# Performance work log

Measured on AMD Instinct MI355X. Metric: run time of the kernel, lower is better.

## Reference

```python
import jax, jax.numpy as jnp
import numpy as np

B, S, D = 4, 2048, 512
H, DK, DV = 8, 64, 64

def setup_inputs() -> dict:
    key = jax.random.key(0)
    ks = jax.random.split(key, 11)
    s = 0.02
    return {
        "q_in": jax.random.normal(ks[0], (B, S, D), jnp.float32),
        "k_in": jax.random.normal(ks[1], (B, S, D), jnp.float32),
        "v_in": jax.random.normal(ks[2], (B, S, D), jnp.float32),
        "Wq": jax.random.normal(ks[3], (H, D, DK), jnp.float32) * s,
        "bq": jax.random.normal(ks[4], (H, DK), jnp.float32) * s,
        "Wk": jax.random.normal(ks[5], (H, D, DK), jnp.float32) * s,
        "bk": jax.random.normal(ks[6], (H, DK), jnp.float32) * s,
        "Wv": jax.random.normal(ks[7], (H, D, DV), jnp.float32) * s,
        "bv": jax.random.normal(ks[8], (H, DV), jnp.float32) * s,
        "Wo": jax.random.normal(ks[9], (H * DV, D), jnp.float32) * s,
        "bo": jax.random.normal(ks[10], (D,), jnp.float32) * s,
    }


def reference(q_in, k_in, v_in, Wq, bq, Wk, bk, Wv, bv, Wo, bo):
    # Per-head Q/K/V projections, batched over heads (same math as the
    # original Python loop over SingleAttention heads).
    q = jnp.einsum("bsd,hdk->bhsk", q_in, Wq) + bq[None, :, None, :]   # [B,H,S,DK]
    k = jnp.einsum("bsd,hdk->bhsk", k_in, Wk) + bk[None, :, None, :]   # [B,H,S,DK]
    v = jnp.einsum("bsd,hdv->bhsv", v_in, Wv) + bv[None, :, None, :]   # [B,H,S,DV]
    scale = 1.0 / jnp.sqrt(jnp.float32(DK))
    scores = jnp.einsum("bhqk,bhsk->bhqs", q, k) * scale               # [B,H,S,S]
    attn = jax.nn.softmax(scores, axis=-1)
    out = jnp.einsum("bhqs,bhsv->bhqv", attn, v)                        # [B,H,S,DV]
    # concat heads along feature dim: [B,S,H*DV]
    concat = out.transpose(0, 2, 1, 3).reshape(B, S, H * DV)
    return concat @ Wo + bo                                             # [B,S,D]
```

## Files before the change

### kernel.cpp

```cpp
#include <hip/hip_runtime.h>
#include <hip/hip_bf16.h>

using bf16 = __hip_bfloat16;
typedef short short8  __attribute__((ext_vector_type(8)));
typedef short short4v __attribute__((ext_vector_type(4)));
typedef float float4v __attribute__((ext_vector_type(4)));
typedef float f32x16  __attribute__((ext_vector_type(16)));
typedef unsigned int uint4v __attribute__((ext_vector_type(4)));

#define MFMA_BF16   __builtin_amdgcn_mfma_f32_16x16x32_bf16
#define MFMA32_BF16 __builtin_amdgcn_mfma_f32_32x32x16_bf16

#define B_  4
#define S_  2048
#define D_  512
#define H_  8
#define DK_ 64


__device__ __forceinline__ short f2bf(float f) {
  bf16 h = __float2bfloat16(f);
  return *reinterpret_cast<short*>(&h);
}

__device__ __forceinline__ unsigned cvtpk(float lo, float hi) {
  unsigned r;
  asm("v_cvt_pk_bf16_f32 %0, %1, %2" : "=v"(r) : "v"(lo), "v"(hi));
  return r;
}

__device__ __forceinline__ void plswap(unsigned& a, unsigned& b) {
  asm("v_permlane32_swap_b32 %0, %1" : "+v"(a), "+v"(b));
}

__device__ __forceinline__ short8 mk8(unsigned v0, unsigned v1, unsigned v2,
                                      unsigned v3) {
  uint4v u;
  u[0] = v0; u[1] = v1; u[2] = v2; u[3] = v3;
  return __builtin_bit_cast(short8, u);
}

__global__ __launch_bounds__(256)
void transpose_w(const float* __restrict__ Wq, const float* __restrict__ Wk,
                 const float* __restrict__ Wv, const float* __restrict__ Wo,
                 short* __restrict__ WqT, short* __restrict__ WkT,
                 short* __restrict__ WvT, short* __restrict__ WoT) {
  __shared__ float tile[64 * 65];
  const int mat = blockIdx.y, t = blockIdx.x, tid = threadIdx.x;
  const float* W = (mat == 0) ? Wq : (mat == 1) ? Wk : (mat == 2) ? Wv : Wo;
  short* T       = (mat == 0) ? WqT : (mat == 1) ? WkT : (mat == 2) ? WvT : WoT;

  size_t sbase, ss, dbase;
  if (mat < 3) {
    int hh = t >> 3, d0 = (t & 7) * 64;
    sbase = (size_t)hh * 32768 + (size_t)d0 * 64;
    ss = 64;
    dbase = (size_t)hh * 64 * 512 + d0;
  } else {
    int n0 = (t >> 3) * 64, k0 = (t & 7) * 64;
    sbase = (size_t)k0 * 512 + n0;
    ss = 512;
    dbase = (size_t)n0 * 512 + k0;
  }

  {
    int r = tid >> 2, c0 = (tid & 3) * 16;
#pragma unroll
    for (int j = 0; j < 4; j++)
      *(float4v*)&tile[r * 65 + c0 + j * 4] =
          *(const float4v*)&W[sbase + (size_t)r * ss + c0 + j * 4];
  }
  __syncthreads();
  {
    int c = tid >> 2, r0 = (tid & 3) * 16;
#pragma unroll
    for (int j = 0; j < 2; j++) {
      short8 s;
#pragma unroll
      for (int u = 0; u < 8; u++) s[u] = f2bf(tile[(r0 + j * 8 + u) * 65 + c]);
      *(short8*)&T[dbase + (size_t)c * 512 + r0 + j * 8] = s;
    }
  }
}

__device__ __forceinline__ void gemm_core(const void* __restrict__ A,
                                          const short* __restrict__ Bt,
                                          int m0, int n0, int fp32,
                                          short* As, short* Bs,
                                          float4v acc[4][4]) {
  const int tid  = threadIdx.x;
  const int lane = tid & 63, wave = tid >> 6;
  const int quad = lane >> 4, l16 = lane & 15;
  const int wm = (wave >> 1) * 64, wn = (wave & 1) * 64;

  for (int k0 = 0; k0 < 512; k0 += 64) {
    __syncthreads();
    if (fp32) {
      const float* Af = (const float*)A;
#pragma unroll
      for (int i = 0; i < 4; i++) {
        int cid = tid + 256 * i;
        int row = cid >> 3, kc = (cid & 7) * 8;
        size_t base = (size_t)(m0 + row) * 512 + k0 + kc;
        float4v f0 = *(const float4v*)&Af[base];
        float4v f1 = *(const float4v*)&Af[base + 4];
        short8 s;
#pragma unroll
        for (int j = 0; j < 4; j++) { s[j] = f2bf(f0[j]); s[j + 4] = f2bf(f1[j]); }
        *(short8*)&As[row * 72 + kc] = s;
        *(short8*)&Bs[row * 72 + kc] =
            *(const short8*)&Bt[(size_t)(n0 + row) * 512 + k0 + kc];
      }
    } else {
      const short* Ab = (const short*)A;
#pragma unroll
      for (int i = 0; i < 4; i++) {
        int cid = tid + 256 * i;
        int row = cid >> 3, kc = (cid & 7) * 8;
        *(short8*)&As[row * 72 + kc] =
            *(const short8*)&Ab[(size_t)(m0 + row) * 512 + k0 + kc];
        *(short8*)&Bs[row * 72 + kc] =
            *(const short8*)&Bt[(size_t)(n0 + row) * 512 + k0 + kc];
      }
    }
    __syncthreads();
#pragma unroll
    for (int ks = 0; ks < 64; ks += 32) {
      short8 af[4], bfr[4];
#pragma unroll
      for (int mi = 0; mi < 4; mi++)
        af[mi] = *(short8*)&As[(wm + mi * 16 + l16) * 72 + ks + quad * 8];
#pragma unroll
      for (int ni = 0; ni < 4; ni++)
        bfr[ni] = *(short8*)&Bs[(wn + ni * 16 + l16) * 72 + ks + quad * 8];
#pragma unroll
      for (int mi = 0; mi < 4; mi++)
#pragma unroll
        for (int ni = 0; ni < 4; ni++)
          acc[mi][ni] = MFMA_BF16(af[mi], bfr[ni], acc[mi][ni], 0, 0, 0);
    }
  }
}

__global__ __launch_bounds__(256, 2)
void qkv_gemm(const float* __restrict__ qin, const float* __restrict__ kin,
              const float* __restrict__ vin,
              const short* __restrict__ WqT, const short* __restrict__ WkT,
              const short* __restrict__ WvT,
              const float* __restrict__ bq, const float* __restrict__ bk,
              const float* __restrict__ bv,
              short* __restrict__ Qp, short* __restrict__ Kp,
              short* __restrict__ Vt) {
  __shared__ __align__(16) short As[128 * 72];
  __shared__ __align__(16) short Bs[128 * 72];
  const int m0 = blockIdx.x * 128, n0 = blockIdx.y * 128;
  const int z = blockIdx.z;
  const float* A    = (z == 0) ? qin : (z == 1) ? kin : vin;
  const short* Bt   = (z == 0) ? WqT : (z == 1) ? WkT : WvT;
  const float* bias = (z == 0) ? bq  : (z == 1) ? bk  : bv;
  const float scale = (z == 0) ? 0.125f * 1.44269504088896f : 1.0f;

  float4v acc[4][4];
#pragma unroll
  for (int mi = 0; mi < 4; mi++)
#pragma unroll
    for (int ni = 0; ni < 4; ni++) acc[mi][ni] = (float4v){0.f, 0.f, 0.f, 0.f};

  gemm_core((const void*)A, Bt, m0, n0, 1, As, Bs, acc);

  const int lane = threadIdx.x & 63, wave = threadIdx.x >> 6;
  const int quad = lane >> 4, l16 = lane & 15;
  const int wm = (wave >> 1) * 64, wn = (wave & 1) * 64;

  if (z < 2) {
    short* out = (z == 0) ? Qp : Kp;
#pragma unroll
    for (int mi = 0; mi < 4; mi++) {
      int m = m0 + wm + mi * 16 + quad * 4;
      int b = m >> 11, s = m & 2047;
#pragma unroll
      for (int ni = 0; ni < 4; ni++) {
        int n = n0 + wn + ni * 16 + l16;
        int h = n >> 6, dk = n & 63;
        float bb = bias[n];
        size_t base = (((size_t)b * H_ + h) * S_ + s) * 64 + dk;
#pragma unroll
        for (int r = 0; r < 4; r++)
          out[base + (size_t)r * 64] = f2bf((acc[mi][ni][r] + bb) * scale);
      }
    }
  } else {
#pragma unroll
    for (int mi = 0; mi < 4; mi++) {
      int m = m0 + wm + mi * 16 + quad * 4;
      int b = m >> 11, s = m & 2047;
#pragma unroll
      for (int ni = 0; ni < 4; ni++) {
        int n = n0 + wn + ni * 16 + l16;
        int h = n >> 6, v = n & 63;
        float bb = bias[n];
        short4v pk;
#pragma unroll
        for (int r = 0; r < 4; r++) pk[r] = f2bf(acc[mi][ni][r] + bb);
        *(short4v*)&Vt[(((size_t)b * H_ + h) * 64 + v) * S_ + s] = pk;
      }
    }
  }
}

__global__ __launch_bounds__(256, 4)
void attn_kernel(const short* __restrict__ Qp, const short* __restrict__ Kp,
                 const short* __restrict__ Vt, short* __restrict__ Ao) {
  __shared__ __align__(16) short Ksh[2][4096];
  __shared__ __align__(16) short Vsh[2][4096];

  const int orig = blockIdx.y * gridDim.x + blockIdx.x;
  const int lb = (orig & 7) * 64 + (orig >> 3);
  const int qt = lb & 15, bh = lb >> 4;
  const int b = bh >> 3, h = bh & 7;

  const int tid = threadIdx.x;
  const int lane = tid & 63, wave = tid >> 6;
  const int l31 = lane & 31, hi = lane >> 5, s7 = l31 & 7;

  const short* Qb = Qp + (size_t)bh * S_ * 64;
  const short* Kb = Kp + (size_t)bh * S_ * 64;
  const short* Vb = Vt + (size_t)bh * 64 * S_;

  short8 qf[4];
  {
    const short* qrow = Qb + (size_t)(qt * 128 + wave * 32 + l31) * 64;
#pragma unroll
    for (int w = 0; w < 4; w++)
      qf[w] = *(const short8*)&qrow[w * 16 + hi * 8];
  }

  const int slot0 = wave * 128 + lane;
  const int kr0 = slot0 >> 3, kc0 = slot0 & 7;
  const int kr1 = kr0 + 8;
  const short* kg0 = Kb + (size_t)kr0 * 64 + ((kc0 ^ (kr0 & 7)) << 3);
  const short* kg1 = Kb + (size_t)kr1 * 64 + ((kc0 ^ (kr1 & 7)) << 3);
  const short* vg0 = Vb + (size_t)kr0 * S_ + ((kc0 ^ (kr0 & 7)) << 3);
  const short* vg1 = Vb + (size_t)kr1 * S_ + ((kc0 ^ (kr1 & 7)) << 3);

#define GLL(g, l) __builtin_amdgcn_global_load_lds(                        \
      (const __attribute__((address_space(1))) void*)(g),                  \
      (__attribute__((address_space(3))) void*)(l), 16, 0, 0)

  f32x16 acc0, acc1;
#pragma unroll
  for (int r = 0; r < 16; r++) { acc0[r] = 0.f; acc1[r] = 0.f; }
  float ls0 = 0.f, ls1 = 0.f;

  {
    short* kd = &Ksh[0][wave * 1024];
    short* vd = &Vsh[0][wave * 1024];
    GLL(kg0, kd); GLL(kg1, kd + 512);
    GLL(vg0, vd); GLL(vg1, vd + 512);
  }
  __syncthreads();

  for (int t = 0; t < 32; t++) {
    const int cur = t & 1;
    if (t < 31) {
      short* kd = &Ksh[cur ^ 1][wave * 1024];
      short* vd = &Vsh[cur ^ 1][wave * 1024];
      GLL(kg0 + (size_t)(t + 1) * 4096, kd);
      GLL(kg1 + (size_t)(t + 1) * 4096, kd + 512);
      GLL(vg0 + (size_t)(t + 1) * 64, vd);
      GLL(vg1 + (size_t)(t + 1) * 64, vd + 512);
    }
    const short* kb = Ksh[cur];
    const short* vs = Vsh[cur];

#pragma unroll
    for (int kt = 0; kt < 2; kt++) {
      f32x16 sa;
#pragma unroll
      for (int r = 0; r < 16; r++) sa[r] = 0.f;
      __builtin_amdgcn_s_setprio(1);
#pragma unroll
      for (int w = 0; w < 4; w++) {
        short8 kf = *(const short8*)&kb[(kt * 32 + l31) * 64 +
                                        (((2 * w + hi) ^ s7) << 3)];
        sa = MFMA32_BF16(kf, qf[w], sa, 0, 0, 0);
      }
      __builtin_amdgcn_s_setprio(0);

      float pv[16];
#pragma unroll
      for (int r = 0; r < 16; r++) pv[r] = exp2f(sa[r]);
#pragma unroll
      for (int r = 0; r < 8; r++) { ls0 += pv[r]; ls1 += pv[r + 8]; }

      unsigned a0 = cvtpk(pv[0], pv[1]),  b0 = cvtpk(pv[4], pv[5]);
      plswap(a0, b0);
      unsigned c0 = cvtpk(pv[2], pv[3]),  d0 = cvtpk(pv[6], pv[7]);
      plswap(c0, d0);
      short8 pa0 = mk8(a0, c0, b0, d0);
      unsigned a1 = cvtpk(pv[8], pv[9]),  b1 = cvtpk(pv[12], pv[13]);
      plswap(a1, b1);
      unsigned c1 = cvtpk(pv[10], pv[11]), d1 = cvtpk(pv[14], pv[15]);
      plswap(c1, d1);
      short8 pa1 = mk8(a1, c1, b1, d1);

      __builtin_amdgcn_s_setprio(1);
      {
        const int kw0 = kt * 2, kw1 = kt * 2 + 1;
        short8 v00 = *(const short8*)&vs[l31 * 64 + (((2 * kw0 + hi) ^ s7) << 3)];
        short8 v10 = *(const short8*)&vs[(32 + l31) * 64 + (((2 * kw0 + hi) ^ s7) << 3)];
        acc0 = MFMA32_BF16(pa0, v00, acc0, 0, 0, 0);
        acc1 = MFMA32_BF16(pa0, v10, acc1, 0, 0, 0);
        short8 v01 = *(const short8*)&vs[l31 * 64 + (((2 * kw1 + hi) ^ s7) << 3)];
        short8 v11 = *(const short8*)&vs[(32 + l31) * 64 + (((2 * kw1 + hi) ^ s7) << 3)];
        acc0 = MFMA32_BF16(pa1, v01, acc0, 0, 0, 0);
        acc1 = MFMA32_BF16(pa1, v11, acc1, 0, 0, 0);
      }
      __builtin_amdgcn_s_setprio(0);
    }
    __syncthreads();
  }
#undef GLL

  float lsum = ls0 + ls1;
  lsum += __shfl_xor(lsum, 32, 64);
  float myrl = 1.0f / lsum;

  const size_t obase =
      ((size_t)b * S_ + (size_t)(qt * 128 + wave * 32)) * D_ + h * 64 + l31;
#pragma unroll
  for (int r = 0; r < 16; r++) {
    int q = (r & 3) + 8 * (r >> 2) + 4 * hi;
    float rl = __shfl(myrl, q, 64);
    Ao[obase + (size_t)q * D_]      = f2bf(acc0[r] * rl);
    Ao[obase + (size_t)q * D_ + 32] = f2bf(acc1[r] * rl);
  }
}

__global__ __launch_bounds__(256, 2)
void out_gemm(const short* __restrict__ A, const short* __restrict__ Bt,
              const float* __restrict__ bias, float* __restrict__ out) {
  __shared__ __align__(16) short As[128 * 72];
  __shared__ __align__(16) short Bs[128 * 72];
  const int m0 = blockIdx.x * 128, n0 = blockIdx.y * 128;

  float4v acc[4][4];
#pragma unroll
  for (int mi = 0; mi < 4; mi++)
#pragma unroll
    for (int ni = 0; ni < 4; ni++) acc[mi][ni] = (float4v){0.f, 0.f, 0.f, 0.f};

  gemm_core((const void*)A, Bt, m0, n0, 0, As, Bs, acc);

  const int lane = threadIdx.x & 63, wave = threadIdx.x >> 6;
  const int quad = lane >> 4, l16 = lane & 15;
  const int wm = (wave >> 1) * 64, wn = (wave & 1) * 64;
#pragma unroll
  for (int mi = 0; mi < 4; mi++) {
    int m = m0 + wm + mi * 16 + quad * 4;
#pragma unroll
    for (int ni = 0; ni < 4; ni++) {
      int n = n0 + wn + ni * 16 + l16;
      float bb = bias[n];
#pragma unroll
      for (int r = 0; r < 4; r++)
        out[(size_t)(m + r) * 512 + n] = acc[mi][ni][r] + bb;
    }
  }
}

extern "C" void kernel_launch(void* const* d_in, const int* in_sizes, int n_in,
                              void* d_out, int out_size, void* d_ws, size_t ws_size,
                              hipStream_t stream) {
  const float* qin = (const float*)d_in[0];
  const float* kin = (const float*)d_in[1];
  const float* vin = (const float*)d_in[2];
  const float* Wq  = (const float*)d_in[3];
  const float* bq  = (const float*)d_in[4];
  const float* Wk  = (const float*)d_in[5];
  const float* bk  = (const float*)d_in[6];
  const float* Wv  = (const float*)d_in[7];
  const float* bv  = (const float*)d_in[8];
  const float* Wo  = (const float*)d_in[9];
  const float* bo  = (const float*)d_in[10];
  float* out = (float*)d_out;
  short* ws  = (short*)d_ws;

  const size_t NTOK = (size_t)B_ * S_ * D_;
  short* Qp  = ws;
  short* Kp  = ws + NTOK;
  short* Vt  = ws + 2 * NTOK;
  short* Ao  = ws + 3 * NTOK;
  short* WqT = ws + 4 * NTOK;
  short* WkT = WqT + 512 * 512;
  short* WvT = WkT + 512 * 512;
  short* WoT = WvT + 512 * 512;

  transpose_w<<<dim3(64, 4), 256, 0, stream>>>(Wq, Wk, Wv, Wo,
                                               WqT, WkT, WvT, WoT);
  qkv_gemm<<<dim3(64, 4, 3), 256, 0, stream>>>(qin, kin, vin, WqT, WkT, WvT,
                                               bq, bk, bv, Qp, Kp, Vt);
  attn_kernel<<<dim3(16, 32), 256, 0, stream>>>(Qp, Kp, Vt, Ao);
  out_gemm<<<dim3(64, 4), 256, 0, stream>>>(Ao, WoT, bo, out);
}
```

Measured before the change: 208.3 us.

## Pre-convert activations to bf16 and stage GEMM tiles via direct global-to-LDS loads

Merges the weight transpose with a new pass that converts q/k/v inputs from fp32 to bf16 into a workspace buffer. The projection and output GEMMs then load bf16 tiles straight into shared memory with global_load_lds, and the padded LDS layout (stride 72) becomes an unpadded stride of 64. This is meant to take the conversion and register staging out of the GEMM inner loop. In exchange it adds a full extra read and write of the activations, and the unpadded layout may cause LDS bank conflicts when fragments are read.

```diff
diff --git a/kernel.cpp b/kernel.cpp
--- a/kernel.cpp
+++ b/kernel.cpp
@@ -17,7 +17,6 @@
 #define H_  8
 #define DK_ 64
 
-
 __device__ __forceinline__ short f2bf(float f) {
   bf16 h = __float2bfloat16(f);
   return *reinterpret_cast<short*>(&h);
@@ -40,13 +39,37 @@
   return __builtin_bit_cast(short8, u);
 }
 
+#define GLL(g, l) __builtin_amdgcn_global_load_lds(                        \
+      (const __attribute__((address_space(1))) void*)(g),                  \
+      (__attribute__((address_space(3))) void*)(l), 16, 0, 0)
+
 __global__ __launch_bounds__(256)
-void transpose_w(const float* __restrict__ Wq, const float* __restrict__ Wk,
-                 const float* __restrict__ Wv, const float* __restrict__ Wo,
-                 short* __restrict__ WqT, short* __restrict__ WkT,
-                 short* __restrict__ WvT, short* __restrict__ WoT) {
+void prep(const float* __restrict__ qin, const float* __restrict__ kin,
+          const float* __restrict__ vin, short* __restrict__ Xb,
+          const float* __restrict__ Wq, const float* __restrict__ Wk,
+          const float* __restrict__ Wv, const float* __restrict__ Wo,
+          short* __restrict__ WqT, short* __restrict__ WkT,
+          short* __restrict__ WvT, short* __restrict__ WoT) {
   __shared__ float tile[64 * 65];
-  const int mat = blockIdx.y, t = blockIdx.x, tid = threadIdx.x;
+  const int bid = blockIdx.x, tid = threadIdx.x;
+  const size_t NTOK = (size_t)B_ * S_ * D_;
+
+  if (bid < 6144) {
+    const int z = bid >> 11, blk = bid & 2047;
+    const float* src = (z == 0) ? qin : (z == 1) ? kin : vin;
+    short* dst = Xb + (size_t)z * NTOK;
+    const size_t base = ((size_t)blk * 256 + tid) * 8;
+    float4v f0 = *(const float4v*)&src[base];
+    float4v f1 = *(const float4v*)&src[base + 4];
+    short8 s;
+#pragma unroll
+    for (int j = 0; j < 4; j++) { s[j] = f2bf(f0[j]); s[j + 4] = f2bf(f1[j]); }
+    *(short8*)&dst[base] = s;
+    return;
+  }
+
+  const int tw = bid - 6144;
+  const int mat = tw >> 6, t = tw & 63;
   const float* W = (mat == 0) ? Wq : (mat == 1) ? Wk : (mat == 2) ? Wv : Wo;
   short* T       = (mat == 0) ? WqT : (mat == 1) ? WkT : (mat == 2) ? WvT : WoT;
 
@@ -83,45 +106,28 @@
   }
 }
 
-__device__ __forceinline__ void gemm_core(const void* __restrict__ A,
-                                          const short* __restrict__ Bt,
-                                          int m0, int n0, int fp32,
-                                          short* As, short* Bs,
-                                          float4v acc[4][4]) {
+__device__ __forceinline__ void gemm_core2(const short* __restrict__ A,
+                                           const short* __restrict__ Bt,
+                                           int m0, int n0,
+                                           short* As, short* Bs,
+                                           float4v acc[4][4]) {
   const int tid  = threadIdx.x;
   const int lane = tid & 63, wave = tid >> 6;
   const int quad = lane >> 4, l16 = lane & 15;
   const int wm = (wave >> 1) * 64, wn = (wave & 1) * 64;
 
+  const int slot = wave * 256 + lane;
+
   for (int k0 = 0; k0 < 512; k0 += 64) {
     __syncthreads();
-    if (fp32) {
-      const float* Af = (const float*)A;
-#pragma unroll
-      for (int i = 0; i < 4; i++) {
-        int cid = tid + 256 * i;
-        int row = cid >> 3, kc = (cid & 7) * 8;
-        size_t base = (size_t)(m0 + row) * 512 + k0 + kc;
-        float4v f0 = *(const float4v*)&Af[base];
-        float4v f1 = *(const float4v*)&Af[base + 4];
-        short8 s;
-#pragma unroll
-        for (int j = 0; j < 4; j++) { s[j] = f2bf(f0[j]); s[j + 4] = f2bf(f1[j]); }
-        *(short8*)&As[row * 72 + kc] = s;
-        *(short8*)&Bs[row * 72 + kc] =
-            *(const short8*)&Bt[(size_t)(n0 + row) * 512 + k0 + kc];
-      }
-    } else {
-      const short* Ab = (const short*)A;
-#pragma unroll
-      for (int i = 0; i < 4; i++) {
-        int cid = tid + 256 * i;
-        int row = cid >> 3, kc = (cid & 7) * 8;
-        *(short8*)&As[row * 72 + kc] =
-            *(const short8*)&Ab[(size_t)(m0 + row) * 512 + k0 + kc];
-        *(short8*)&Bs[row * 72 + kc] =
-            *(const short8*)&Bt[(size_t)(n0 + row) * 512 + k0 + kc];
-      }
+#pragma unroll
+    for (int i = 0; i < 4; i++) {
+      int s = slot + i * 64;
+      int row = s >> 3, c8 = (s & 7) * 8;
+      GLL(&A[(size_t)(m0 + row) * 512 + k0 + c8],
+          &As[(size_t)(wave * 256 + i * 64) * 8]);
+      GLL(&Bt[(size_t)(n0 + row) * 512 + k0 + c8],
+          &Bs[(size_t)(wave * 256 + i * 64) * 8]);
     }
     __syncthreads();
 #pragma unroll
@@ -129,10 +135,10 @@
       short8 af[4], bfr[4];
 #pragma unroll
       for (int mi = 0; mi < 4; mi++)
-        af[mi] = *(short8*)&As[(wm + mi * 16 + l16) * 72 + ks + quad * 8];
+        af[mi] = *(short8*)&As[(wm + mi * 16 + l16) * 64 + ks + quad * 8];
 #pragma unroll
       for (int ni = 0; ni < 4; ni++)
-        bfr[ni] = *(short8*)&Bs[(wn + ni * 16 + l16) * 72 + ks + quad * 8];
+        bfr[ni] = *(short8*)&Bs[(wn + ni * 16 + l16) * 64 + ks + quad * 8];
 #pragma unroll
       for (int mi = 0; mi < 4; mi++)
 #pragma unroll
@@ -143,19 +149,19 @@
 }
 
 __global__ __launch_bounds__(256, 2)
-void qkv_gemm(const float* __restrict__ qin, const float* __restrict__ kin,
-              const float* __restrict__ vin,
+void qkv_gemm(const short* __restrict__ Xb,
               const short* __restrict__ WqT, const short* __restrict__ WkT,
               const short* __restrict__ WvT,
               const float* __restrict__ bq, const float* __restrict__ bk,
               const float* __restrict__ bv,
               short* __restrict__ Qp, short* __restrict__ Kp,
               short* __restrict__ Vt) {
-  __shared__ __align__(16) short As[128 * 72];
-  __shared__ __align__(16) short Bs[128 * 72];
+  __shared__ __align__(16) short As[128 * 64];
+  __shared__ __align__(16) short Bs[128 * 64];
   const int m0 = blockIdx.x * 128, n0 = blockIdx.y * 128;
   const int z = blockIdx.z;
-  const float* A    = (z == 0) ? qin : (z == 1) ? kin : vin;
+  const size_t NTOK = (size_t)B_ * S_ * D_;
+  const short* A    = Xb + (size_t)z * NTOK;
   const short* Bt   = (z == 0) ? WqT : (z == 1) ? WkT : WvT;
   const float* bias = (z == 0) ? bq  : (z == 1) ? bk  : bv;
   const float scale = (z == 0) ? 0.125f * 1.44269504088896f : 1.0f;
@@ -166,7 +172,7 @@
 #pragma unroll
     for (int ni = 0; ni < 4; ni++) acc[mi][ni] = (float4v){0.f, 0.f, 0.f, 0.f};
 
-  gemm_core((const void*)A, Bt, m0, n0, 1, As, Bs, acc);
+  gemm_core2(A, Bt, m0, n0, As, Bs, acc);
 
   const int lane = threadIdx.x & 63, wave = threadIdx.x >> 6;
   const int quad = lane >> 4, l16 = lane & 15;
@@ -242,10 +248,6 @@
   const short* kg1 = Kb + (size_t)kr1 * 64 + ((kc0 ^ (kr1 & 7)) << 3);
   const short* vg0 = Vb + (size_t)kr0 * S_ + ((kc0 ^ (kr0 & 7)) << 3);
   const short* vg1 = Vb + (size_t)kr1 * S_ + ((kc0 ^ (kr1 & 7)) << 3);
-
-#define GLL(g, l) __builtin_amdgcn_global_load_lds(                        \
-      (const __attribute__((address_space(1))) void*)(g),                  \
-      (__attribute__((address_space(3))) void*)(l), 16, 0, 0)
 
   f32x16 acc0, acc1;
 #pragma unroll
@@ -320,7 +322,6 @@
     }
     __syncthreads();
   }
-#undef GLL
 
   float lsum = ls0 + ls1;
   lsum += __shfl_xor(lsum, 32, 64);
@@ -340,8 +341,8 @@
 __global__ __launch_bounds__(256, 2)
 void out_gemm(const short* __restrict__ A, const short* __restrict__ Bt,
               const float* __restrict__ bias, float* __restrict__ out) {
-  __shared__ __align__(16) short As[128 * 72];
-  __shared__ __align__(16) short Bs[128 * 72];
+  __shared__ __align__(16) short As[128 * 64];
+  __shared__ __align__(16) short Bs[128 * 64];
   const int m0 = blockIdx.x * 128, n0 = blockIdx.y * 128;
 
   float4v acc[4][4];
@@ -350,7 +351,7 @@
 #pragma unroll
     for (int ni = 0; ni < 4; ni++) acc[mi][ni] = (float4v){0.f, 0.f, 0.f, 0.f};
 
-  gemm_core((const void*)A, Bt, m0, n0, 0, As, Bs, acc);
+  gemm_core2(A, Bt, m0, n0, As, Bs, acc);
 
   const int lane = threadIdx.x & 63, wave = threadIdx.x >> 6;
   const int quad = lane >> 4, l16 = lane & 15;
@@ -395,10 +396,11 @@
   short* WkT = WqT + 512 * 512;
   short* WvT = WkT + 512 * 512;
   short* WoT = WvT + 512 * 512;
-
-  transpose_w<<<dim3(64, 4), 256, 0, stream>>>(Wq, Wk, Wv, Wo,
-                                               WqT, WkT, WvT, WoT);
-  qkv_gemm<<<dim3(64, 4, 3), 256, 0, stream>>>(qin, kin, vin, WqT, WkT, WvT,
+  short* Xb  = WoT + 512 * 512;
+
+  prep<<<dim3(6400), 256, 0, stream>>>(qin, kin, vin, Xb, Wq, Wk, Wv, Wo,
+                                       WqT, WkT, WvT, WoT);
+  qkv_gemm<<<dim3(64, 4, 3), 256, 0, stream>>>(Xb, WqT, WkT, WvT,
                                                bq, bk, bv, Qp, Kp, Vt);
   attn_kernel<<<dim3(16, 32), 256, 0, stream>>>(Qp, Kp, Vt, Ao);
   out_gemm<<<dim3(64, 4), 256, 0, stream>>>(Ao, WoT, bo, out);
```

Result: no change. 205.4 us (-1.4%).
